# Optimization experiments

Measured on AMD Instinct MI355X. Metric: run time of the kernel, lower is better.

The kernel has to match this reference:

```python
import jax, jax.numpy as jnp
import numpy as np

HIDDEN = 512
HEADS = 8
HEAD_DIM = HIDDEN // HEADS   # 64
MAN_DIM = 256                # manifold_dim = hidden_dim // 2
SCALE = HEAD_DIM ** -0.5


def _c(re, im):
    return jax.lax.complex(re, im)


def setup_inputs() -> dict:
    key = jax.random.key(0)
    ks = jax.random.split(key, 13)
    def w(k, shape, fan_in):
        return (jax.random.normal(k, shape, dtype=jnp.float32) / np.sqrt(fan_in)).astype(jnp.float32)
    B, S = 2, 2048
    return {
        "x": jax.random.normal(ks[0], (B, S, HIDDEN), dtype=jnp.float32),
        "Wq_re": w(ks[1], (HIDDEN, HIDDEN), HIDDEN), "Wq_im": w(ks[2], (HIDDEN, HIDDEN), HIDDEN),
        "Wk_re": w(ks[3], (HIDDEN, HIDDEN), HIDDEN), "Wk_im": w(ks[4], (HIDDEN, HIDDEN), HIDDEN),
        "Wv_re": w(ks[5], (HIDDEN, HIDDEN), HIDDEN), "Wv_im": w(ks[6], (HIDDEN, HIDDEN), HIDDEN),
        "Wm_re": w(ks[7], (HEAD_DIM, MAN_DIM), HEAD_DIM), "Wm_im": w(ks[8], (HEAD_DIM, MAN_DIM), HEAD_DIM),
        "Wmi_re": w(ks[9], (MAN_DIM, HEAD_DIM), MAN_DIM), "Wmi_im": w(ks[10], (MAN_DIM, HEAD_DIM), MAN_DIM),
        "Wo_re": w(ks[11], (HIDDEN, HIDDEN), HIDDEN), "Wo_im": w(ks[12], (HIDDEN, HIDDEN), HIDDEN),
    }


def reference(x, Wq_re, Wq_im, Wk_re, Wk_im, Wv_re, Wv_im,
              Wm_re, Wm_im, Wmi_re, Wmi_im, Wo_re, Wo_im):
    B, S, D = x.shape
    # quantum state preparation: cast to complex, L2-normalize along last dim
    xc = x.astype(jnp.complex64)
    norm = jnp.linalg.norm(xc, axis=-1, keepdims=True)
    xc = xc / norm

    Wq, Wk, Wv = _c(Wq_re, Wq_im), _c(Wk_re, Wk_im), _c(Wv_re, Wv_im)
    Wm, Wmi, Wo = _c(Wm_re, Wm_im), _c(Wmi_re, Wmi_im), _c(Wo_re, Wo_im)

    def heads(t):  # [B,S,D] -> [B,H,S,head_dim]
        return t.reshape(B, S, HEADS, HEAD_DIM).transpose(0, 2, 1, 3)

    q = heads(xc @ Wq)
    k = heads(xc @ Wk)
    v = heads(xc @ Wv)

    # project each head onto the manifold (complex linear)
    qm = jnp.einsum('bhsd,dm->bhsm', q, Wm)
    km = jnp.einsum('bhsd,dm->bhsm', k, Wm)
    vm = jnp.einsum('bhsd,dm->bhsm', v, Wm)

    # Hermitian inner product attention scores; softmax over real part
    scores = jnp.einsum('bhqm,bhkm->bhqk', qm, jnp.conj(km)) * SCALE
    attn = jax.nn.softmax(scores.real, axis=-1).astype(jnp.complex64)

    outm = jnp.einsum('bhqk,bhkm->bhqm', attn, vm)
    out = jnp.einsum('bhsm,md->bhsd', outm, Wmi)        # back to head_dim
    out = out.transpose(0, 2, 1, 3).reshape(B, S, D)    # merge heads
    out = out @ Wo
    # return real/imag stacked as float32 (complex64 output -> [B,S,D,2])
    return jnp.stack([out.real, out.imag], axis=-1)
```

## Files before the change

kernel.cpp:

```cpp
#include <hip/hip_runtime.h>
#include <hip/hip_bf16.h>
#include <stdint.h>


typedef __attribute__((ext_vector_type(8))) short bf16x8;
typedef __attribute__((ext_vector_type(4))) float f32x4;

#define QSCALE 0.18033688011112042f

__device__ __forceinline__ unsigned short f2b(float f) {
    union { float f; unsigned int u; } v; v.f = f;
    unsigned int r = v.u + 0x7fffu + ((v.u >> 16) & 1u);
    return (unsigned short)(r >> 16);
}

__device__ __forceinline__ unsigned int cvtpk(float a, float b) {
    union { __hip_bfloat162 h; unsigned int u; } v;
    v.h = __float22bfloat162_rn(make_float2(a, b));
    return v.u;
}

__device__ __forceinline__ void ld16(void* lds, const void* g) {
    __builtin_amdgcn_global_load_lds(
        (__attribute__((address_space(1))) unsigned int*)(g),
        (__attribute__((address_space(3))) unsigned int*)(lds), 16, 0, 0);
}

__global__ __launch_bounds__(256) void k_norm(const float* __restrict__ x,
                                              unsigned short* __restrict__ xn) {
    int row  = blockIdx.x * 4 + (threadIdx.x >> 6);
    int lane = threadIdx.x & 63;
    const float4* xr = (const float4*)(x + (size_t)row * 512);
    float4 a = xr[lane], b = xr[lane + 64];
    float s = a.x*a.x + a.y*a.y + a.z*a.z + a.w*a.w
            + b.x*b.x + b.y*b.y + b.z*b.z + b.w*b.w;
    #pragma unroll
    for (int m = 1; m < 64; m <<= 1) s += __shfl_xor(s, m, 64);
    float inv = 1.0f / sqrtf(s);
    ushort4 o;
    o.x = f2b(a.x*inv); o.y = f2b(a.y*inv); o.z = f2b(a.z*inv); o.w = f2b(a.w*inv);
    *(ushort4*)&xn[(size_t)row*512 + lane*4] = o;
    o.x = f2b(b.x*inv); o.y = f2b(b.y*inv); o.z = f2b(b.z*inv); o.w = f2b(b.w*inv);
    *(ushort4*)&xn[(size_t)row*512 + 256 + lane*4] = o;
}

__global__ __launch_bounds__(256) void k_trans(
        const float* __restrict__ s0, const float* __restrict__ s1,
        const float* __restrict__ s2, const float* __restrict__ s3,
        const float* __restrict__ s4, const float* __restrict__ s5,
        const float* __restrict__ s6, const float* __restrict__ s7,
        float* __restrict__ d0, float* __restrict__ d1,
        float* __restrict__ d2, float* __restrict__ d3,
        float* __restrict__ d4, float* __restrict__ d5,
        float* __restrict__ d6, float* __restrict__ d7) {
    __shared__ float tile[64][65];
    int bid = blockIdx.x;
    const float* src; float* dst; int R, C, tr, tc;
    if (bid < 384) {
        int mat = bid >> 6, tl = bid & 63;
        src = (mat==0)?s0:(mat==1)?s1:(mat==2)?s2:(mat==3)?s3:(mat==4)?s4:s5;
        dst = (mat==0)?d0:(mat==1)?d1:(mat==2)?d2:(mat==3)?d3:(mat==4)?d4:d5;
        R = 512; C = 512; tr = tl >> 3; tc = tl & 7;
    } else {
        int mat = (bid - 384) >> 2, tl = (bid - 384) & 3;
        src = mat ? s7 : s6; dst = mat ? d7 : d6;
        R = 64; C = 256; tr = 0; tc = tl;
    }
    int r0 = tr * 64, c0 = tc * 64;
    int tx = threadIdx.x & 63, ty = threadIdx.x >> 6;
    #pragma unroll
    for (int i = 0; i < 16; i++) {
        int r = ty + i*4;
        tile[r][tx] = src[(size_t)(r0 + r)*C + c0 + tx];
    }
    __syncthreads();
    #pragma unroll
    for (int i = 0; i < 16; i++) {
        int r = ty + i*4;
        dst[(size_t)(c0 + r)*R + r0 + tx] = tile[tx][r];
    }
}

__global__ __launch_bounds__(256) void k_gh(const float* __restrict__ Wm_re, const float* __restrict__ Wm_im,
                                            const float* __restrict__ WmT_re, const float* __restrict__ WmT_im,
                                            const float* __restrict__ Wmi_re, const float* __restrict__ Wmi_im,
                                            float* __restrict__ GH) {
    int id = blockIdx.x * 256 + threadIdx.x;
    int mat = id >> 12;
    int a = (id >> 6) & 63, c = id & 63;
    float s = 0.f;
    if (mat < 2) {
        for (int m = 0; m < 256; m++) {
            float ar = Wm_re[a*256+m], ai = Wm_im[a*256+m];
            float br = WmT_re[m*64+c], bi = WmT_im[m*64+c];
            s += (mat == 0) ? (ar*br + ai*bi) : (ai*br - ar*bi);
        }
        GH[id] = s;
    } else {
        for (int m = 0; m < 256; m++) {
            float ar = Wm_re[a*256+m], ai = Wm_im[a*256+m];
            float br = Wmi_re[m*64+c], bi = Wmi_im[m*64+c];
            s += (mat == 2) ? (ar*br - ai*bi) : (ar*bi + ai*br);
        }
        GH[mat*4096 + c*64 + a] = s;
    }
}

__global__ __launch_bounds__(256) void k_packqkv(
        const float* __restrict__ WqT_re, const float* __restrict__ WqT_im,
        const float* __restrict__ WkT_re, const float* __restrict__ WkT_im,
        const float* __restrict__ WvT_re, const float* __restrict__ WvT_im,
        const float* __restrict__ GH, unsigned short* __restrict__ WqkvT) {
    int id = blockIdx.x * 256 + threadIdx.x;
    int n = id >> 9, k = id & 511;
    float val;
    if (n < 1024) {
        int h = n >> 7, part = (n >> 6) & 1, j = n & 63;
        const float* Gr = GH;
        const float* Gi = GH + 4096;
        const float* qr = WqT_re + (size_t)(h*64)*512 + k;
        const float* qi = WqT_im + (size_t)(h*64)*512 + k;
        float s = 0.f;
        if (part == 0) { for (int d = 0; d < 64; d++) s += qr[d*512]*Gr[d*64+j] - qi[d*512]*Gi[d*64+j]; }
        else           { for (int d = 0; d < 64; d++) s += qr[d*512]*Gi[d*64+j] + qi[d*512]*Gr[d*64+j]; }
        val = s * QSCALE;
    } else if (n < 2048) {
        int m = n - 1024; int h = m >> 7, part = (m >> 6) & 1, j = m & 63;
        val = (part ? WkT_im : WkT_re)[(size_t)(h*64+j)*512 + k];
    } else {
        int m = n - 2048; int h = m >> 7, part = (m >> 6) & 1, j = m & 63;
        val = (part ? WvT_im : WvT_re)[(size_t)(h*64+j)*512 + k];
    }
    WqkvT[id] = f2b(val);
}

__global__ __launch_bounds__(256) void k_packwo(
        const float* __restrict__ Wo_re, const float* __restrict__ Wo_im,
        const float* __restrict__ GH, unsigned short* __restrict__ Wbig) {
    int id = blockIdx.x * 256 + threadIdx.x;
    int np = id >> 10, kk = id & 1023;
    int c = np >> 1, p = np & 1;
    int h = kk >> 7, pp = (kk >> 6) & 1, d = kk & 63;
    const float* HrT = GH + 2*4096;
    const float* HiT = GH + 3*4096;
    float s = 0.f;
    if (p == pp) {
        for (int j = 0; j < 64; j++) {
            float hr = HrT[j*64+d], hi = HiT[j*64+d];
            float wr = Wo_re[(size_t)(h*64+j)*512 + c];
            float wi = Wo_im[(size_t)(h*64+j)*512 + c];
            s += hr*wr - hi*wi;
        }
    } else {
        for (int j = 0; j < 64; j++) {
            float hr = HrT[j*64+d], hi = HiT[j*64+d];
            float wr = Wo_re[(size_t)(h*64+j)*512 + c];
            float wi = Wo_im[(size_t)(h*64+j)*512 + c];
            s += hr*wi + hi*wr;
        }
        if (p == 0) s = -s;
    }
    Wbig[(size_t)np*1024 + kk] = f2b(s);
}

template<int MODE, int MT>
__global__ __launch_bounds__(256, 2) void k_gemm(
        const unsigned short* __restrict__ Ain, const unsigned short* __restrict__ Btin,
        void* __restrict__ Cout, unsigned short* __restrict__ Vt, int K) {
    __shared__ __align__(16) unsigned short Al[MT*32];
    __shared__ __align__(16) unsigned short Bl[128*32];
    const int t = threadIdx.x;
    const int wave = t >> 6, lane = t & 63, quad = lane >> 4, l16 = lane & 15;
    const int wr = wave >> 1, wc = wave & 1;

    const unsigned short* A;
    const unsigned short* Bt;
    unsigned short* Cb = nullptr;
    int m0, n0;
    if (MODE == 0) {
        if (blockIdx.y < 16) {
            A = Ain; Bt = Btin;
            m0 = blockIdx.x * 128; n0 = blockIdx.y * 128;
            Cb = (unsigned short*)Cout;
        } else {
            int idx = (blockIdx.y - 16) * 32 + blockIdx.x;
            int b = idx >> 7, mt = (idx >> 4) & 7, nt = idx & 15;
            A  = Btin + 2048*512;
            Bt = Ain + (size_t)b*2048*512;
            m0 = mt * 128; n0 = nt * 128;
            Cb = Vt + (size_t)b*1024*2048;
        }
    } else {
        A = Ain; Bt = Btin;
        m0 = blockIdx.x * MT; n0 = blockIdx.y * 128;
    }

    f32x4 acc[MT/32][4] = {};
    for (int kt = 0; kt < K; kt += 32) {
        #pragma unroll
        for (int i = 0; i < MT/64; i++) {
            int g = t + i*256, r = g >> 2, gr = g & 3;
            ld16(&Al[g*8], &A[(size_t)(m0 + r)*K + kt + gr*8]);
        }
        #pragma unroll
        for (int i = 0; i < 2; i++) {
            int g = t + i*256, r = g >> 2, gr = g & 3;
            ld16(&Bl[g*8], &Bt[(size_t)(n0 + r)*K + kt + gr*8]);
        }
        __syncthreads();
        bf16x8 af[MT/32], bfr[4];
        #pragma unroll
        for (int rt = 0; rt < MT/32; rt++)
            af[rt] = *(const bf16x8*)&Al[(wr*(MT/2) + rt*16 + l16)*32 + quad*8];
        #pragma unroll
        for (int ct = 0; ct < 4; ct++)
            bfr[ct] = *(const bf16x8*)&Bl[(wc*64 + ct*16 + l16)*32 + quad*8];
        #pragma unroll
        for (int rt = 0; rt < MT/32; rt++)
            #pragma unroll
            for (int ct = 0; ct < 4; ct++)
                acc[rt][ct] = __builtin_amdgcn_mfma_f32_16x16x32_bf16(af[rt], bfr[ct], acc[rt][ct], 0, 0, 0);
        __syncthreads();
    }
    #pragma unroll
    for (int rt = 0; rt < MT/32; rt++) {
        int row = m0 + wr*(MT/2) + rt*16 + quad*4;
        #pragma unroll
        for (int ct = 0; ct < 4; ct++) {
            int col = n0 + wc*64 + ct*16 + l16;
            if (MODE == 0) {
                unsigned int u01 = cvtpk(acc[rt][ct][0], acc[rt][ct][1]);
                unsigned int u23 = cvtpk(acc[rt][ct][2], acc[rt][ct][3]);
                Cb[(size_t)(row+0)*2048 + col] = (unsigned short)(u01);
                Cb[(size_t)(row+1)*2048 + col] = (unsigned short)(u01 >> 16);
                Cb[(size_t)(row+2)*2048 + col] = (unsigned short)(u23);
                Cb[(size_t)(row+3)*2048 + col] = (unsigned short)(u23 >> 16);
            } else {
                float* C = (float*)Cout;
                #pragma unroll
                for (int r = 0; r < 4; r++)
                    C[(size_t)(row + r)*1024 + col] = acc[rt][ct][r];
            }
        }
    }
}

__global__ __launch_bounds__(256, 2) void k_attn(
        const unsigned short* __restrict__ QK,
        const unsigned short* __restrict__ Vt,
        unsigned short* __restrict__ O) {
    __shared__ __align__(16) unsigned short Kl[8192];
    __shared__ __align__(16) unsigned short Vl[8192];
    __shared__ __align__(16) unsigned short Pl[4608];

    const int t = threadIdx.x, wave = t >> 6, lane = t & 63, quad = lane >> 4, l16 = lane & 15;
    const int bh = blockIdx.y, b = bh >> 3, h = bh & 7;
    const int tok0 = b*2048 + blockIdx.x*64;

    #pragma unroll
    for (int i = 0; i < 4; i++) {
        int g = t + i*256, ks = g >> 8, q = (g >> 2) & 63, gr = g & 3;
        ld16(&Kl[g*8], &QK[(size_t)(tok0 + q)*2048 + h*128 + ks*32 + gr*8]);
    }
    __syncthreads();
    bf16x8 qf[4];
    #pragma unroll
    for (int ks = 0; ks < 4; ks++)
        qf[ks] = *(const bf16x8*)&Kl[ks*2048 + (wave*16 + l16)*32 + quad*8];
    __syncthreads();

    f32x4 Oacc[8] = {};
    float ls[4] = {0.f, 0.f, 0.f, 0.f};

    for (int kt = 0; kt < 2048; kt += 64) {
        #pragma unroll
        for (int i = 0; i < 4; i++) {
            int g = t + i*256, ks = g >> 8, key = (g >> 2) & 63, gr = g & 3;
            ld16(&Kl[g*8], &QK[(size_t)(b*2048 + kt + key)*2048 + 1024 + h*128 + ks*32 + gr*8]);
        }
        #pragma unroll
        for (int i = 0; i < 4; i++) {
            int g = t + i*256, ks2 = g >> 9, d = (g >> 2) & 127, gr = g & 3;
            ld16(&Vl[g*8], &Vt[(size_t)(b*1024 + h*128 + d)*2048 + kt + ks2*32 + gr*8]);
        }
        __syncthreads();

        f32x4 S[4] = {};
        #pragma unroll
        for (int ks = 0; ks < 4; ks++) {
            #pragma unroll
            for (int ct = 0; ct < 4; ct++) {
                bf16x8 kf = *(const bf16x8*)&Kl[ks*2048 + (ct*16 + l16)*32 + quad*8];
                S[ct] = __builtin_amdgcn_mfma_f32_16x16x32_bf16(qf[ks], kf, S[ct], 0, 0, 0);
            }
        }
        #pragma unroll
        for (int ct = 0; ct < 4; ct++) {
            #pragma unroll
            for (int r = 0; r < 4; r++) {
                float p = exp2f(S[ct][r]);
                S[ct][r] = p;
                ls[r] += p;
            }
            int q = wave*16 + quad*4;
            int base = (ct >> 1)*2304 + (ct & 1)*16 + l16;
            unsigned int u01 = cvtpk(S[ct][0], S[ct][1]);
            unsigned int u23 = cvtpk(S[ct][2], S[ct][3]);
            Pl[base + (q+0)*36] = (unsigned short)(u01);
            Pl[base + (q+1)*36] = (unsigned short)(u01 >> 16);
            Pl[base + (q+2)*36] = (unsigned short)(u23);
            Pl[base + (q+3)*36] = (unsigned short)(u23 >> 16);
        }
        #pragma unroll
        for (int ks2 = 0; ks2 < 2; ks2++) {
            bf16x8 pf = *(const bf16x8*)&Pl[ks2*2304 + (wave*16 + l16)*36 + quad*8];
            #pragma unroll
            for (int dt = 0; dt < 8; dt++) {
                bf16x8 vf = *(const bf16x8*)&Vl[ks2*4096 + (dt*16 + l16)*32 + quad*8];
                Oacc[dt] = __builtin_amdgcn_mfma_f32_16x16x32_bf16(pf, vf, Oacc[dt], 0, 0, 0);
            }
        }
        __syncthreads();
    }

    #pragma unroll
    for (int r = 0; r < 4; r++) {
        float s = ls[r];
        #pragma unroll
        for (int m = 1; m < 16; m <<= 1) s += __shfl_xor(s, m, 64);
        ls[r] = 1.0f / s;
    }
    int tok = tok0 + wave*16 + quad*4;
    #pragma unroll
    for (int dt = 0; dt < 8; dt++) {
        int col = h*128 + dt*16 + l16;
        unsigned int u01 = cvtpk(Oacc[dt][0]*ls[0], Oacc[dt][1]*ls[1]);
        unsigned int u23 = cvtpk(Oacc[dt][2]*ls[2], Oacc[dt][3]*ls[3]);
        O[(size_t)(tok+0)*1024 + col] = (unsigned short)(u01);
        O[(size_t)(tok+1)*1024 + col] = (unsigned short)(u01 >> 16);
        O[(size_t)(tok+2)*1024 + col] = (unsigned short)(u23);
        O[(size_t)(tok+3)*1024 + col] = (unsigned short)(u23 >> 16);
    }
}

extern "C" void kernel_launch(void* const* d_in, const int* in_sizes, int n_in,
                              void* d_out, int out_size, void* d_ws, size_t ws_size,
                              hipStream_t stream) {
    (void)in_sizes; (void)n_in; (void)out_size; (void)ws_size;
    const float* x      = (const float*)d_in[0];
    const float* Wq_re  = (const float*)d_in[1];
    const float* Wq_im  = (const float*)d_in[2];
    const float* Wk_re  = (const float*)d_in[3];
    const float* Wk_im  = (const float*)d_in[4];
    const float* Wv_re  = (const float*)d_in[5];
    const float* Wv_im  = (const float*)d_in[6];
    const float* Wm_re  = (const float*)d_in[7];
    const float* Wm_im  = (const float*)d_in[8];
    const float* Wmi_re = (const float*)d_in[9];
    const float* Wmi_im = (const float*)d_in[10];
    const float* Wo_re  = (const float*)d_in[11];
    const float* Wo_im  = (const float*)d_in[12];

    char* ws = (char*)d_ws;
    unsigned short* xn    = (unsigned short*)(ws);
    unsigned short* WqkvT = (unsigned short*)(ws + (4u << 20));
    unsigned short* Wbig  = (unsigned short*)(ws + (7u << 20));
    float*          GH    = (float*)         (ws + (9u << 20));
    float*          WmT_re= (float*)         (ws + (9u << 20) + (64u << 10));
    float*          WmT_im= (float*)         (ws + (9u << 20) + (128u << 10));
    unsigned short* QK    = (unsigned short*)(ws + (10u << 20));
    unsigned short* Vt    = (unsigned short*)(ws + (26u << 20));
    unsigned short* Obuf  = (unsigned short*)(ws + (34u << 20));
    float* WqT_re = (float*)(ws + (10u << 20));
    float* WqT_im = (float*)(ws + (11u << 20));
    float* WkT_re = (float*)(ws + (12u << 20));
    float* WkT_im = (float*)(ws + (13u << 20));
    float* WvT_re = (float*)(ws + (14u << 20));
    float* WvT_im = (float*)(ws + (15u << 20));

    k_norm      <<<dim3(1024), dim3(256), 0, stream>>>(x, xn);
    k_trans     <<<dim3(392),  dim3(256), 0, stream>>>(
        Wq_re, Wq_im, Wk_re, Wk_im, Wv_re, Wv_im, Wm_re, Wm_im,
        WqT_re, WqT_im, WkT_re, WkT_im, WvT_re, WvT_im, WmT_re, WmT_im);
    k_gh        <<<dim3(64),   dim3(256), 0, stream>>>(Wm_re, Wm_im, WmT_re, WmT_im, Wmi_re, Wmi_im, GH);
    k_packqkv   <<<dim3(6144), dim3(256), 0, stream>>>(WqT_re, WqT_im, WkT_re, WkT_im, WvT_re, WvT_im, GH, WqkvT);
    k_packwo    <<<dim3(4096), dim3(256), 0, stream>>>(Wo_re, Wo_im, GH, Wbig);
    k_gemm<0,128><<<dim3(32, 24), dim3(256), 0, stream>>>(xn, WqkvT, (void*)QK, Vt, 512);
    k_attn      <<<dim3(32, 16), dim3(256), 0, stream>>>(QK, Vt, Obuf);
    k_gemm<1,64> <<<dim3(64, 8), dim3(256), 0, stream>>>(Obuf, Wbig, d_out, nullptr, 1024);
}
```

Measured before the change: 271.4 us.

## Merge prep/pack kernels and double-buffer attention with 128-query tiles

Combines norm+transpose into one launch and the two weight-pack kernels into one, cutting launch count. The attention kernel now processes 128 queries per block (two row tiles per wave) so each staged K/V tile is reused twice as much, and it double-buffers K/V tiles in LDS so the next tile's global loads overlap with the current tile's MFMAs. This doubles LDS and register use per block, which can lower occupancy. The attention grid is also halved to 256 blocks, which may underfill the GPU.

```diff
diff --git a/kernel.cpp b/kernel.cpp
--- a/kernel.cpp
+++ b/kernel.cpp
@@ -26,25 +26,8 @@
         (__attribute__((address_space(3))) unsigned int*)(lds), 16, 0, 0);
 }
 
-__global__ __launch_bounds__(256) void k_norm(const float* __restrict__ x,
-                                              unsigned short* __restrict__ xn) {
-    int row  = blockIdx.x * 4 + (threadIdx.x >> 6);
-    int lane = threadIdx.x & 63;
-    const float4* xr = (const float4*)(x + (size_t)row * 512);
-    float4 a = xr[lane], b = xr[lane + 64];
-    float s = a.x*a.x + a.y*a.y + a.z*a.z + a.w*a.w
-            + b.x*b.x + b.y*b.y + b.z*b.z + b.w*b.w;
-    #pragma unroll
-    for (int m = 1; m < 64; m <<= 1) s += __shfl_xor(s, m, 64);
-    float inv = 1.0f / sqrtf(s);
-    ushort4 o;
-    o.x = f2b(a.x*inv); o.y = f2b(a.y*inv); o.z = f2b(a.z*inv); o.w = f2b(a.w*inv);
-    *(ushort4*)&xn[(size_t)row*512 + lane*4] = o;
-    o.x = f2b(b.x*inv); o.y = f2b(b.y*inv); o.z = f2b(b.z*inv); o.w = f2b(b.w*inv);
-    *(ushort4*)&xn[(size_t)row*512 + 256 + lane*4] = o;
-}
-
-__global__ __launch_bounds__(256) void k_trans(
+__global__ __launch_bounds__(256) void k_prep(
+        const float* __restrict__ x, unsigned short* __restrict__ xn,
         const float* __restrict__ s0, const float* __restrict__ s1,
         const float* __restrict__ s2, const float* __restrict__ s3,
         const float* __restrict__ s4, const float* __restrict__ s5,
@@ -54,7 +37,24 @@
         float* __restrict__ d4, float* __restrict__ d5,
         float* __restrict__ d6, float* __restrict__ d7) {
     __shared__ float tile[64][65];
-    int bid = blockIdx.x;
+    if (blockIdx.x < 1024) {
+        int row  = blockIdx.x * 4 + (threadIdx.x >> 6);
+        int lane = threadIdx.x & 63;
+        const float4* xr = (const float4*)(x + (size_t)row * 512);
+        float4 a = xr[lane], b = xr[lane + 64];
+        float s = a.x*a.x + a.y*a.y + a.z*a.z + a.w*a.w
+                + b.x*b.x + b.y*b.y + b.z*b.z + b.w*b.w;
+        #pragma unroll
+        for (int m = 1; m < 64; m <<= 1) s += __shfl_xor(s, m, 64);
+        float inv = 1.0f / sqrtf(s);
+        ushort4 o;
+        o.x = f2b(a.x*inv); o.y = f2b(a.y*inv); o.z = f2b(a.z*inv); o.w = f2b(a.w*inv);
+        *(ushort4*)&xn[(size_t)row*512 + lane*4] = o;
+        o.x = f2b(b.x*inv); o.y = f2b(b.y*inv); o.z = f2b(b.z*inv); o.w = f2b(b.w*inv);
+        *(ushort4*)&xn[(size_t)row*512 + 256 + lane*4] = o;
+        return;
+    }
+    int bid = blockIdx.x - 1024;
     const float* src; float* dst; int R, C, tr, tc;
     if (bid < 384) {
         int mat = bid >> 6, tl = bid & 63;
@@ -106,61 +106,61 @@
     }
 }
 
-__global__ __launch_bounds__(256) void k_packqkv(
+__global__ __launch_bounds__(256) void k_pack(
         const float* __restrict__ WqT_re, const float* __restrict__ WqT_im,
         const float* __restrict__ WkT_re, const float* __restrict__ WkT_im,
         const float* __restrict__ WvT_re, const float* __restrict__ WvT_im,
-        const float* __restrict__ GH, unsigned short* __restrict__ WqkvT) {
-    int id = blockIdx.x * 256 + threadIdx.x;
-    int n = id >> 9, k = id & 511;
-    float val;
-    if (n < 1024) {
-        int h = n >> 7, part = (n >> 6) & 1, j = n & 63;
-        const float* Gr = GH;
-        const float* Gi = GH + 4096;
-        const float* qr = WqT_re + (size_t)(h*64)*512 + k;
-        const float* qi = WqT_im + (size_t)(h*64)*512 + k;
+        const float* __restrict__ Wo_re,  const float* __restrict__ Wo_im,
+        const float* __restrict__ GH,
+        unsigned short* __restrict__ WqkvT, unsigned short* __restrict__ Wbig) {
+    if (blockIdx.x < 6144) {
+        int id = blockIdx.x * 256 + threadIdx.x;
+        int n = id >> 9, k = id & 511;
+        float val;
+        if (n < 1024) {
+            int h = n >> 7, part = (n >> 6) & 1, j = n & 63;
+            const float* Gr = GH;
+            const float* Gi = GH + 4096;
+            const float* qr = WqT_re + (size_t)(h*64)*512 + k;
+            const float* qi = WqT_im + (size_t)(h*64)*512 + k;
+            float s = 0.f;
+            if (part == 0) { for (int d = 0; d < 64; d++) s += qr[d*512]*Gr[d*64+j] - qi[d*512]*Gi[d*64+j]; }
+            else           { for (int d = 0; d < 64; d++) s += qr[d*512]*Gi[d*64+j] + qi[d*512]*Gr[d*64+j]; }
+            val = s * QSCALE;
+        } else if (n < 2048) {
+            int m = n - 1024; int h = m >> 7, part = (m >> 6) & 1, j = m & 63;
+            val = (part ? WkT_im : WkT_re)[(size_t)(h*64+j)*512 + k];
+        } else {
+            int m = n - 2048; int h = m >> 7, part = (m >> 6) & 1, j = m & 63;
+            val = (part ? WvT_im : WvT_re)[(size_t)(h*64+j)*512 + k];
+        }
+        WqkvT[id] = f2b(val);
+    } else {
+        int id = (blockIdx.x - 6144) * 256 + threadIdx.x;
+        int np = id >> 10, kk = id & 1023;
+        int c = np >> 1, p = np & 1;
+        int h = kk >> 7, pp = (kk >> 6) & 1, d = kk & 63;
+        const float* HrT = GH + 2*4096;
+        const float* HiT = GH + 3*4096;
         float s = 0.f;
-        if (part == 0) { for (int d = 0; d < 64; d++) s += qr[d*512]*Gr[d*64+j] - qi[d*512]*Gi[d*64+j]; }
-        else           { for (int d = 0; d < 64; d++) s += qr[d*512]*Gi[d*64+j] + qi[d*512]*Gr[d*64+j]; }
-        val = s * QSCALE;
-    } else if (n < 2048) {
-        int m = n - 1024; int h = m >> 7, part = (m >> 6) & 1, j = m & 63;
-        val = (part ? WkT_im : WkT_re)[(size_t)(h*64+j)*512 + k];
-    } else {
-        int m = n - 2048; int h = m >> 7, part = (m >> 6) & 1, j = m & 63;
-        val = (part ? WvT_im : WvT_re)[(size_t)(h*64+j)*512 + k];
-    }
-    WqkvT[id] = f2b(val);
-}
-
-__global__ __launch_bounds__(256) void k_packwo(
-        const float* __restrict__ Wo_re, const float* __restrict__ Wo_im,
-        const float* __restrict__ GH, unsigned short* __restrict__ Wbig) {
-    int id = blockIdx.x * 256 + threadIdx.x;
-    int np = id >> 10, kk = id & 1023;
-    int c = np >> 1, p = np & 1;
-    int h = kk >> 7, pp = (kk >> 6) & 1, d = kk & 63;
-    const float* HrT = GH + 2*4096;
-    const float* HiT = GH + 3*4096;
-    float s = 0.f;
-    if (p == pp) {
-        for (int j = 0; j < 64; j++) {
-            float hr = HrT[j*64+d], hi = HiT[j*64+d];
-            float wr = Wo_re[(size_t)(h*64+j)*512 + c];
-            float wi = Wo_im[(size_t)(h*64+j)*512 + c];
-            s += hr*wr - hi*wi;
-        }
-    } else {
-        for (int j = 0; j < 64; j++) {
-            float hr = HrT[j*64+d], hi = HiT[j*64+d];
-            float wr = Wo_re[(size_t)(h*64+j)*512 + c];
-            float wi = Wo_im[(size_t)(h*64+j)*512 + c];
-            s += hr*wi + hi*wr;
-        }
-        if (p == 0) s = -s;
-    }
-    Wbig[(size_t)np*1024 + kk] = f2b(s);
+        if (p == pp) {
+            for (int j = 0; j < 64; j++) {
+                float hr = HrT[j*64+d], hi = HiT[j*64+d];
+                float wr = Wo_re[(size_t)(h*64+j)*512 + c];
+                float wi = Wo_im[(size_t)(h*64+j)*512 + c];
+                s += hr*wr - hi*wi;
+            }
+        } else {
+            for (int j = 0; j < 64; j++) {
+                float hr = HrT[j*64+d], hi = HiT[j*64+d];
+                float wr = Wo_re[(size_t)(h*64+j)*512 + c];
+                float wi = Wo_im[(size_t)(h*64+j)*512 + c];
+                s += hr*wi + hi*wr;
+            }
+            if (p == 0) s = -s;
+        }
+        Wbig[(size_t)np*1024 + kk] = f2b(s);
+    }
 }
 
 template<int MODE, int MT>
@@ -249,97 +249,116 @@
         const unsigned short* __restrict__ QK,
         const unsigned short* __restrict__ Vt,
         unsigned short* __restrict__ O) {
-    __shared__ __align__(16) unsigned short Kl[8192];
-    __shared__ __align__(16) unsigned short Vl[8192];
-    __shared__ __align__(16) unsigned short Pl[4608];
+    __shared__ __align__(16) unsigned short Kl[2][8192];
+    __shared__ __align__(16) unsigned short Vl[2][8192];
+    __shared__ __align__(16) unsigned short Pl[9216];
 
     const int t = threadIdx.x, wave = t >> 6, lane = t & 63, quad = lane >> 4, l16 = lane & 15;
-    const int bh = blockIdx.y, b = bh >> 3, h = bh & 7;
-    const int tok0 = b*2048 + blockIdx.x*64;
-
-    #pragma unroll
-    for (int i = 0; i < 4; i++) {
-        int g = t + i*256, ks = g >> 8, q = (g >> 2) & 63, gr = g & 3;
-        ld16(&Kl[g*8], &QK[(size_t)(tok0 + q)*2048 + h*128 + ks*32 + gr*8]);
+    const int bh = blockIdx.x, b = bh >> 3, h = bh & 7;
+    const int tok0 = b*2048 + blockIdx.y*128;
+
+    bf16x8 qf[2][4];
+    #pragma unroll
+    for (int rt = 0; rt < 2; rt++)
+        #pragma unroll
+        for (int ks = 0; ks < 4; ks++)
+            qf[rt][ks] = *(const bf16x8*)&QK[(size_t)(tok0 + wave*32 + rt*16 + l16)*2048 + h*128 + ks*32 + quad*8];
+
+    const int key = t >> 2, gr = t & 3;
+    const unsigned short* kp  = QK + (size_t)(b*2048 + key)*2048 + 1024 + h*128 + gr*8;
+    const unsigned short* vp0 = Vt + (size_t)(b*1024 + h*128 + key)*2048 + gr*8;
+    const unsigned short* vp1 = Vt + (size_t)(b*1024 + h*128 + 64 + key)*2048 + gr*8;
+
+    f32x4 Oacc[2][8] = {};
+    float ls[2][4] = {};
+
+    {
+        size_t ko = 0;
+        #pragma unroll
+        for (int i = 0; i < 4; i++) ld16(&Kl[0][(i*256 + t)*8], kp + ko + i*32);
+        #pragma unroll
+        for (int i = 0; i < 4; i++) ld16(&Vl[0][(i*256 + t)*8], ((i & 1) ? vp1 : vp0) + (i >> 1)*32);
     }
     __syncthreads();
-    bf16x8 qf[4];
-    #pragma unroll
-    for (int ks = 0; ks < 4; ks++)
-        qf[ks] = *(const bf16x8*)&Kl[ks*2048 + (wave*16 + l16)*32 + quad*8];
-    __syncthreads();
-
-    f32x4 Oacc[8] = {};
-    float ls[4] = {0.f, 0.f, 0.f, 0.f};
-
-    for (int kt = 0; kt < 2048; kt += 64) {
-        #pragma unroll
-        for (int i = 0; i < 4; i++) {
-            int g = t + i*256, ks = g >> 8, key = (g >> 2) & 63, gr = g & 3;
-            ld16(&Kl[g*8], &QK[(size_t)(b*2048 + kt + key)*2048 + 1024 + h*128 + ks*32 + gr*8]);
-        }
-        #pragma unroll
-        for (int i = 0; i < 4; i++) {
-            int g = t + i*256, ks2 = g >> 9, d = (g >> 2) & 127, gr = g & 3;
-            ld16(&Vl[g*8], &Vt[(size_t)(b*1024 + h*128 + d)*2048 + kt + ks2*32 + gr*8]);
+
+    for (int it = 0; it < 32; it++) {
+        const int cur = it & 1;
+        if (it < 31) {
+            int kt = (it + 1) * 64;
+            size_t ko = (size_t)kt * 2048;
+            #pragma unroll
+            for (int i = 0; i < 4; i++) ld16(&Kl[cur^1][(i*256 + t)*8], kp + ko + i*32);
+            #pragma unroll
+            for (int i = 0; i < 4; i++) ld16(&Vl[cur^1][(i*256 + t)*8], ((i & 1) ? vp1 : vp0) + kt + (i >> 1)*32);
+        }
+
+        f32x4 S[2][4] = {};
+        #pragma unroll
+        for (int ks = 0; ks < 4; ks++) {
+            #pragma unroll
+            for (int ct = 0; ct < 4; ct++) {
+                bf16x8 kf = *(const bf16x8*)&Kl[cur][ks*2048 + (ct*16 + l16)*32 + quad*8];
+                #pragma unroll
+                for (int rt = 0; rt < 2; rt++)
+                    S[rt][ct] = __builtin_amdgcn_mfma_f32_16x16x32_bf16(qf[rt][ks], kf, S[rt][ct], 0, 0, 0);
+            }
+        }
+        #pragma unroll
+        for (int rt = 0; rt < 2; rt++) {
+            #pragma unroll
+            for (int ct = 0; ct < 4; ct++) {
+                float p0 = exp2f(S[rt][ct][0]), p1 = exp2f(S[rt][ct][1]);
+                float p2 = exp2f(S[rt][ct][2]), p3 = exp2f(S[rt][ct][3]);
+                ls[rt][0] += p0; ls[rt][1] += p1; ls[rt][2] += p2; ls[rt][3] += p3;
+                int q = wave*32 + rt*16 + quad*4;
+                int base = (ct >> 1)*4608 + (ct & 1)*16 + l16;
+                unsigned int u01 = cvtpk(p0, p1);
+                unsigned int u23 = cvtpk(p2, p3);
+                Pl[base + (q+0)*36] = (unsigned short)(u01);
+                Pl[base + (q+1)*36] = (unsigned short)(u01 >> 16);
+                Pl[base + (q+2)*36] = (unsigned short)(u23);
+                Pl[base + (q+3)*36] = (unsigned short)(u23 >> 16);
+            }
+        }
+        #pragma unroll
+        for (int ks2 = 0; ks2 < 2; ks2++) {
+            bf16x8 pf[2];
+            #pragma unroll
+            for (int rt = 0; rt < 2; rt++)
+                pf[rt] = *(const bf16x8*)&Pl[ks2*4608 + (wave*32 + rt*16 + l16)*36 + quad*8];
+            #pragma unroll
+            for (int dt = 0; dt < 8; dt++) {
+                bf16x8 vf = *(const bf16x8*)&Vl[cur][ks2*4096 + (dt*16 + l16)*32 + quad*8];
+                #pragma unroll
+                for (int rt = 0; rt < 2; rt++)
+                    Oacc[rt][dt] = __builtin_amdgcn_mfma_f32_16x16x32_bf16(pf[rt], vf, Oacc[rt][dt], 0, 0, 0);
+            }
         }
         __syncthreads();
-
-        f32x4 S[4] = {};
-        #pragma unroll
-        for (int ks = 0; ks < 4; ks++) {
-            #pragma unroll
-            for (int ct = 0; ct < 4; ct++) {
-                bf16x8 kf = *(const bf16x8*)&Kl[ks*2048 + (ct*16 + l16)*32 + quad*8];
-                S[ct] = __builtin_amdgcn_mfma_f32_16x16x32_bf16(qf[ks], kf, S[ct], 0, 0, 0);
-            }
-        }
-        #pragma unroll
-        for (int ct = 0; ct < 4; ct++) {
-            #pragma unroll
-            for (int r = 0; r < 4; r++) {
-                float p = exp2f(S[ct][r]);
-                S[ct][r] = p;
-                ls[r] += p;
-            }
-            int q = wave*16 + quad*4;
-            int base = (ct >> 1)*2304 + (ct & 1)*16 + l16;
-            unsigned int u01 = cvtpk(S[ct][0], S[ct][1]);
-            unsigned int u23 = cvtpk(S[ct][2], S[ct][3]);
-            Pl[base + (q+0)*36] = (unsigned short)(u01);
-            Pl[base + (q+1)*36] = (unsigned short)(u01 >> 16);
-            Pl[base + (q+2)*36] = (unsigned short)(u23);
-            Pl[base + (q+3)*36] = (unsigned short)(u23 >> 16);
-        }
-        #pragma unroll
-        for (int ks2 = 0; ks2 < 2; ks2++) {
-            bf16x8 pf = *(const bf16x8*)&Pl[ks2*2304 + (wave*16 + l16)*36 + quad*8];
-            #pragma unroll
-            for (int dt = 0; dt < 8; dt++) {
-                bf16x8 vf = *(const bf16x8*)&Vl[ks2*4096 + (dt*16 + l16)*32 + quad*8];
-                Oacc[dt] = __builtin_amdgcn_mfma_f32_16x16x32_bf16(pf, vf, Oacc[dt], 0, 0, 0);
-            }
-        }
-        __syncthreads();
-    }
-
-    #pragma unroll
-    for (int r = 0; r < 4; r++) {
-        float s = ls[r];
-        #pragma unroll
-        for (int m = 1; m < 16; m <<= 1) s += __shfl_xor(s, m, 64);
-        ls[r] = 1.0f / s;
-    }
-    int tok = tok0 + wave*16 + quad*4;
-    #pragma unroll
-    for (int dt = 0; dt < 8; dt++) {
-        int col = h*128 + dt*16 + l16;
-        unsigned int u01 = cvtpk(Oacc[dt][0]*ls[0], Oacc[dt][1]*ls[1]);
-        unsigned int u23 = cvtpk(Oacc[dt][2]*ls[2], Oacc[dt][3]*ls[3]);
-        O[(size_t)(tok+0)*1024 + col] = (unsigned short)(u01);
-        O[(size_t)(tok+1)*1024 + col] = (unsigned short)(u01 >> 16);
-        O[(size_t)(tok+2)*1024 + col] = (unsigned short)(u23);
-        O[(size_t)(tok+3)*1024 + col] = (unsigned short)(u23 >> 16);
+    }
+
+    #pragma unroll
+    for (int rt = 0; rt < 2; rt++)
+        #pragma unroll
+        for (int r = 0; r < 4; r++) {
+            float s = ls[rt][r];
+            #pragma unroll
+            for (int m = 1; m < 16; m <<= 1) s += __shfl_xor(s, m, 64);
+            ls[rt][r] = 1.0f / s;
+        }
+    #pragma unroll
+    for (int rt = 0; rt < 2; rt++) {
+        int tok = tok0 + wave*32 + rt*16 + quad*4;
+        #pragma unroll
+        for (int dt = 0; dt < 8; dt++) {
+            int col = h*128 + dt*16 + l16;
+            unsigned int u01 = cvtpk(Oacc[rt][dt][0]*ls[rt][0], Oacc[rt][dt][1]*ls[rt][1]);
+            unsigned int u23 = cvtpk(Oacc[rt][dt][2]*ls[rt][2], Oacc[rt][dt][3]*ls[rt][3]);
+            O[(size_t)(tok+0)*1024 + col] = (unsigned short)(u01);
+            O[(size_t)(tok+1)*1024 + col] = (unsigned short)(u01 >> 16);
+            O[(size_t)(tok+2)*1024 + col] = (unsigned short)(u23);
+            O[(size_t)(tok+3)*1024 + col] = (unsigned short)(u23 >> 16);
+        }
     }
 }
 
@@ -378,14 +397,14 @@
     float* WvT_re = (float*)(ws + (14u << 20));
     float* WvT_im = (float*)(ws + (15u << 20));
 
-    k_norm      <<<dim3(1024), dim3(256), 0, stream>>>(x, xn);
-    k_trans     <<<dim3(392),  dim3(256), 0, stream>>>(
+    k_prep      <<<dim3(1416), dim3(256), 0, stream>>>(
+        x, xn,
         Wq_re, Wq_im, Wk_re, Wk_im, Wv_re, Wv_im, Wm_re, Wm_im,
         WqT_re, WqT_im, WkT_re, WkT_im, WvT_re, WvT_im, WmT_re, WmT_im);
     k_gh        <<<dim3(64),   dim3(256), 0, stream>>>(Wm_re, Wm_im, WmT_re, WmT_im, Wmi_re, Wmi_im, GH);
-    k_packqkv   <<<dim3(6144), dim3(256), 0, stream>>>(WqT_re, WqT_im, WkT_re, WkT_im, WvT_re, WvT_im, GH, WqkvT);
-    k_packwo    <<<dim3(4096), dim3(256), 0, stream>>>(Wo_re, Wo_im, GH, Wbig);
+    k_pack      <<<dim3(10240),dim3(256), 0, stream>>>(
+        WqT_re, WqT_im, WkT_re, WkT_im, WvT_re, WvT_im, Wo_re, Wo_im, GH, WqkvT, Wbig);
     k_gemm<0,128><<<dim3(32, 24), dim3(256), 0, stream>>>(xn, WqkvT, (void*)QK, Vt, 512);
-    k_attn      <<<dim3(32, 16), dim3(256), 0, stream>>>(QK, Vt, Obuf);
+    k_attn      <<<dim3(16, 16), dim3(256), 0, stream>>>(QK, Vt, Obuf);
     k_gemm<1,64> <<<dim3(64, 8), dim3(256), 0, stream>>>(Obuf, Wbig, d_out, nullptr, 1024);
 }
```

Result: no change. 271.6 us (+0.1%).
